# Optimization experiments

Measured on AMD Instinct MI355X. Metric: run time of the kernel, lower is better.

Reference implementation:

```python
import jax, jax.numpy as jnp
import numpy as np

N = 50000
E = 800000
IN_C, HID_C, OUT_C = 512, 128, 256


def setup_inputs() -> dict:
    key = jax.random.key(0)
    k1, k2, k3, k4, k5, k6 = jax.random.split(key, 6)
    x = jax.random.normal(k1, (N, IN_C), dtype=jnp.float32)
    edge_index = jax.random.randint(k2, (2, E), 0, N, dtype=jnp.int64)
    # Linear weights stored torch-style as [out, in]; bias per layer
    w1 = jax.random.normal(k3, (HID_C, IN_C), dtype=jnp.float32) * (1.0 / np.sqrt(IN_C))
    b1 = jax.random.normal(k4, (HID_C,), dtype=jnp.float32) * 0.02
    w2 = jax.random.normal(k5, (OUT_C, HID_C), dtype=jnp.float32) * (1.0 / np.sqrt(HID_C))
    b2 = jax.random.normal(k6, (OUT_C,), dtype=jnp.float32) * 0.02
    return {"x": x, "edge_index": edge_index, "w1": w1, "b1": b1, "w2": w2, "b2": b2}


def gcn_conv(x, edge_index, w, b):
    # x: [N, Cin], w: [Cout, Cin] (torch Linear layout), b: [Cout]
    h = x @ w.T                              # [N, Cout]
    src, dst = edge_index[0], edge_index[1]
    msgs = h[src]                            # gather: [E, Cout]
    agg = jax.ops.segment_sum(msgs, dst, num_segments=h.shape[0])  # scatter_add
    return agg + b


def reference(x, edge_index, w1, b1, w2, b2):
    h = gcn_conv(x, edge_index, w1, b1)
    h = jax.nn.relu(h)
    out = gcn_conv(h, edge_index, w2, b2)
    return out
```

## Files before the change

kernel.cpp:

```cpp
#include <hip/hip_runtime.h>

#define NN 50000
#define EE 800000
#define INC 512
#define HIDC 128
#define OUTC 256
#define CAP 64
#define OV_CAP 65536
#define BUILD_BLOCKS 196
#define GB1 782

typedef __attribute__((ext_vector_type(8))) short bf16x8;
typedef __attribute__((ext_vector_type(4))) float f32x4;

__device__ __forceinline__ short f2bf(float f) {
    unsigned u = __float_as_uint(f);
    unsigned r = u + 0x7fff + ((u >> 16) & 1);
    return (short)(r >> 16);
}
__device__ __forceinline__ float bf2f(short s) {
    return __uint_as_float(((unsigned)(unsigned short)s) << 16);
}

template<bool IN_BF16, bool ADDBIAS, bool OUT_BF16>
__device__ __forceinline__ void gemm_core(
    const void* __restrict__ Av, const float* __restrict__ B,
    const float* __restrict__ bias, void* __restrict__ Cv,
    int M, int Nc, int K, int bx, int by,
    short As[64][72], short Bs[128][72])
{
    int tid = threadIdx.x;
    int lane = tid & 63, wave = tid >> 6;
    int row0 = bx * 64, col0 = by * 128;
    int wm = (wave & 1) * 32, wn = (wave >> 1) * 64;
    int l16 = lane & 15, quad = lane >> 4;

    f32x4 acc[2][4];
#pragma unroll
    for (int i = 0; i < 2; i++)
#pragma unroll
        for (int j = 0; j < 4; j++) acc[i][j] = {0.f, 0.f, 0.f, 0.f};

    for (int k0 = 0; k0 < K; k0 += 64) {
        if (IN_BF16) {
            const short* A = (const short*)Av;
#pragma unroll
            for (int w = 0; w < 2; w++) {
                int f = tid + w * 256;
                int rr = f >> 3, c8 = f & 7;
                int gr = row0 + rr;
                bf16x8 v = {0, 0, 0, 0, 0, 0, 0, 0};
                if (gr < M) v = *(const bf16x8*)&A[(long)gr * K + k0 + c8 * 8];
                *(bf16x8*)&As[rr][c8 * 8] = v;
            }
        } else {
            const float* A = (const float*)Av;
#pragma unroll
            for (int w = 0; w < 4; w++) {
                int f = tid + w * 256;
                int rr = f >> 4, c4 = f & 15;
                int gr = row0 + rr;
                float4 v = make_float4(0.f, 0.f, 0.f, 0.f);
                if (gr < M) v = *(const float4*)&A[(long)gr * K + k0 + c4 * 4];
                short4 s;
                s.x = f2bf(v.x); s.y = f2bf(v.y); s.z = f2bf(v.z); s.w = f2bf(v.w);
                *(short4*)&As[rr][c4 * 4] = s;
            }
        }
#pragma unroll
        for (int w = 0; w < 8; w++) {
            int f = tid + w * 256;
            int rr = f >> 4, c4 = f & 15;
            float4 v = *(const float4*)&B[(long)(col0 + rr) * K + k0 + c4 * 4];
            short4 s;
            s.x = f2bf(v.x); s.y = f2bf(v.y); s.z = f2bf(v.z); s.w = f2bf(v.w);
            *(short4*)&Bs[rr][c4 * 4] = s;
        }
        __syncthreads();

#pragma unroll
        for (int kk = 0; kk < 64; kk += 32) {
            bf16x8 af[2], bfr[4];
#pragma unroll
            for (int i = 0; i < 2; i++)
                af[i] = *(const bf16x8*)&As[wm + i * 16 + l16][kk + quad * 8];
#pragma unroll
            for (int j = 0; j < 4; j++)
                bfr[j] = *(const bf16x8*)&Bs[wn + j * 16 + l16][kk + quad * 8];
#pragma unroll
            for (int i = 0; i < 2; i++)
#pragma unroll
                for (int j = 0; j < 4; j++)
                    acc[i][j] = __builtin_amdgcn_mfma_f32_16x16x32_bf16(
                        af[i], bfr[j], acc[i][j], 0, 0, 0);
        }
        __syncthreads();
    }

#pragma unroll
    for (int i = 0; i < 2; i++) {
#pragma unroll
        for (int rr = 0; rr < 4; rr++) {
            int grow = row0 + wm + i * 16 + quad * 4 + rr;
            if (grow < M) {
#pragma unroll
                for (int j = 0; j < 4; j++) {
                    int gcol = col0 + wn + j * 16 + l16;
                    float v = acc[i][j][rr];
                    if (ADDBIAS) v += bias[gcol];
                    if (OUT_BF16)
                        ((short*)Cv)[(long)grow * Nc + gcol] = f2bf(v);
                    else
                        ((float*)Cv)[(long)grow * Nc + gcol] = v;
                }
            }
        }
    }
}

__global__ __launch_bounds__(256) void fat_build_gemm1(
    const int* __restrict__ ei, int* __restrict__ cnt,
    unsigned short* __restrict__ bucket, int* __restrict__ ovcnt,
    int* __restrict__ ovlist,
    const float* __restrict__ x, const float* __restrict__ w1,
    short* __restrict__ h)
{
    __shared__ short As[64][72];
    __shared__ short Bs[128][72];

    if (blockIdx.x < BUILD_BLOCKS) {
        int t = threadIdx.x;
        long base = ((long)blockIdx.x * 256 + t) * 16;
        if (base + 16 <= EE) {
            int4 sv[4], dv[4];
#pragma unroll
            for (int q = 0; q < 4; q++) {
                sv[q] = *(const int4*)&ei[base + q * 4];
                dv[q] = *(const int4*)&ei[EE + base + q * 4];
            }
            const int* sp = (const int*)sv;
            const int* dp = (const int*)dv;
#pragma unroll
            for (int k = 0; k < 16; k++) {
                int src = sp[k], dst = dp[k];
                int pos = atomicAdd(&cnt[dst], 1);
                if (pos < CAP) bucket[(long)dst * CAP + pos] = (unsigned short)src;
                else {
                    int o = atomicAdd(ovcnt, 1);
                    if (o < OV_CAP) { ovlist[o * 2] = src; ovlist[o * 2 + 1] = dst; }
                }
            }
        } else {
            for (int k = 0; k < 16; k++) {
                long e = base + k;
                if (e < EE) {
                    int src = ei[e], dst = ei[EE + e];
                    int pos = atomicAdd(&cnt[dst], 1);
                    if (pos < CAP) bucket[(long)dst * CAP + pos] = (unsigned short)src;
                    else {
                        int o = atomicAdd(ovcnt, 1);
                        if (o < OV_CAP) { ovlist[o * 2] = src; ovlist[o * 2 + 1] = dst; }
                    }
                }
            }
        }
    } else {
        gemm_core<false, false, true>(x, w1, nullptr, h, NN, HIDC, INC,
                                      blockIdx.x - BUILD_BLOCKS, 0, As, Bs);
    }
}

__global__ __launch_bounds__(256) void gemm2_k(
    const short* __restrict__ r2, const float* __restrict__ w2,
    const float* __restrict__ b2, float* __restrict__ out)
{
    __shared__ short As[64][72];
    __shared__ short Bs[128][72];
    gemm_core<true, true, false>(r2, w2, b2, out, NN, OUTC, HIDC,
                                 blockIdx.x, blockIdx.y, As, Bs);
}

template<bool RELU>
__global__ __launch_bounds__(256) void gather_k(
    const short* __restrict__ hsrc, const unsigned short* __restrict__ bucket,
    const int* __restrict__ cnt, const float* __restrict__ bias,
    float* __restrict__ aggf, short* __restrict__ rout)
{
    int t = threadIdx.x;
    int node = blockIdx.x * 16 + (t >> 4);
    int c8 = t & 15;
    if (node >= NN) return;
    int m = cnt[node]; if (m > CAP) m = CAP;
    const unsigned short* bk = bucket + (long)node * CAP;
    float acc[8];
#pragma unroll
    for (int k = 0; k < 8; k++) acc[k] = 0.f;
    int j = 0;
    for (; j + 4 <= m; j += 4) {
        int s0 = bk[j], s1 = bk[j + 1], s2 = bk[j + 2], s3 = bk[j + 3];
        bf16x8 v0 = *(const bf16x8*)&hsrc[((long)s0 << 7) + c8 * 8];
        bf16x8 v1 = *(const bf16x8*)&hsrc[((long)s1 << 7) + c8 * 8];
        bf16x8 v2 = *(const bf16x8*)&hsrc[((long)s2 << 7) + c8 * 8];
        bf16x8 v3 = *(const bf16x8*)&hsrc[((long)s3 << 7) + c8 * 8];
#pragma unroll
        for (int k = 0; k < 8; k++)
            acc[k] += bf2f(v0[k]) + bf2f(v1[k]) + bf2f(v2[k]) + bf2f(v3[k]);
    }
    for (; j < m; j++) {
        int s0 = bk[j];
        bf16x8 v0 = *(const bf16x8*)&hsrc[((long)s0 << 7) + c8 * 8];
#pragma unroll
        for (int k = 0; k < 8; k++) acc[k] += bf2f(v0[k]);
    }
    if (RELU) {
        *(float4*)&aggf[((long)node << 7) + c8 * 8] =
            make_float4(acc[0], acc[1], acc[2], acc[3]);
        *(float4*)&aggf[((long)node << 7) + c8 * 8 + 4] =
            make_float4(acc[4], acc[5], acc[6], acc[7]);
        bf16x8 o;
#pragma unroll
        for (int k = 0; k < 8; k++)
            o[k] = f2bf(fmaxf(acc[k] + bias[c8 * 8 + k], 0.f));
        *(bf16x8*)&rout[((long)node << 7) + c8 * 8] = o;
    } else {
        bf16x8 o;
#pragma unroll
        for (int k = 0; k < 8; k++) o[k] = f2bf(acc[k]);
        *(bf16x8*)&rout[((long)node << 7) + c8 * 8] = o;
    }
}

__global__ __launch_bounds__(128) void ovfix1_k(
    const short* __restrict__ h, const float* __restrict__ b1,
    const int* __restrict__ ovcnt, const int* __restrict__ ovlist,
    float* __restrict__ agg1, short* __restrict__ r)
{
    int n = *ovcnt; if (n > OV_CAP) n = OV_CAP;
    int c = threadIdx.x;
    for (int i = 0; i < n; i++) {
        int src = ovlist[i * 2], dst = ovlist[i * 2 + 1];
        agg1[(long)dst * 128 + c] += bf2f(h[(long)src * 128 + c]);
    }
    __syncthreads();
    for (int i = 0; i < n; i++) {
        int dst = ovlist[i * 2 + 1];
        r[(long)dst * 128 + c] =
            f2bf(fmaxf(agg1[(long)dst * 128 + c] + b1[c], 0.f));
    }
}

__global__ __launch_bounds__(128) void ovfix2_k(
    const short* __restrict__ r, const unsigned short* __restrict__ bucket,
    const int* __restrict__ cnt, const int* __restrict__ ovcnt,
    const int* __restrict__ ovlist, short* __restrict__ r2)
{
    int n = *ovcnt; if (n > OV_CAP) n = OV_CAP;
    int c = threadIdx.x;
    for (int i = 0; i < n; i++) {
        int dst = ovlist[i * 2 + 1];
        bool dup = false;
        for (int i2 = 0; i2 < i; i2++)
            if (ovlist[i2 * 2 + 1] == dst) { dup = true; break; }
        if (dup) continue;
        int m = cnt[dst]; if (m > CAP) m = CAP;
        const unsigned short* bk = bucket + (long)dst * CAP;
        float acc = 0.f;
        for (int j = 0; j < m; j++)
            acc += bf2f(r[(long)bk[j] * 128 + c]);
        for (int i2 = 0; i2 < n; i2++)
            if (ovlist[i2 * 2 + 1] == dst)
                acc += bf2f(r[(long)ovlist[i2 * 2] * 128 + c]);
        r2[(long)dst * 128 + c] = f2bf(acc);
    }
}

extern "C" void kernel_launch(void* const* d_in, const int* in_sizes, int n_in,
                              void* d_out, int out_size, void* d_ws, size_t ws_size,
                              hipStream_t stream) {
    const float* x  = (const float*)d_in[0];
    const int*   ei = (const int*)d_in[1];
    const float* w1 = (const float*)d_in[2];
    const float* b1 = (const float*)d_in[3];
    const float* w2 = (const float*)d_in[4];
    const float* b2 = (const float*)d_in[5];
    float* out = (float*)d_out;

    char* ws = (char*)d_ws;
    size_t off = 0;
    short* h    = (short*)(ws + off); off += (size_t)NN * HIDC * 2;
    float* agg1 = (float*)(ws + off); off += (size_t)NN * HIDC * 4;
    short* r    = (short*)(ws + off); off += (size_t)NN * HIDC * 2;
    short* r2   = (short*)(ws + off); off += (size_t)NN * HIDC * 2;
    unsigned short* bucket = (unsigned short*)(ws + off);
    off += (size_t)NN * CAP * 2;
    int* cnt    = (int*)(ws + off);   off += (size_t)NN * 4;
    int* ovcnt  = (int*)(ws + off);   off += 256;
    int* ovlist = (int*)(ws + off);   off += (size_t)OV_CAP * 2 * 4;

    hipMemsetAsync(cnt, 0, (size_t)NN * 4 + 4, stream);

    dim3 blk(256);

    fat_build_gemm1<<<dim3(BUILD_BLOCKS + GB1), blk, 0, stream>>>(
        ei, cnt, bucket, ovcnt, ovlist, x, w1, h);

    gather_k<true><<<dim3(3125), blk, 0, stream>>>(h, bucket, cnt, b1, agg1, r);
    ovfix1_k<<<dim3(1), dim3(128), 0, stream>>>(h, b1, ovcnt, ovlist, agg1, r);

    gather_k<false><<<dim3(3125), blk, 0, stream>>>(r, bucket, cnt, nullptr, nullptr, r2);
    ovfix2_k<<<dim3(1), dim3(128), 0, stream>>>(r, bucket, cnt, ovcnt, ovlist, r2);

    gemm2_k<<<dim3(GB1, 2), blk, 0, stream>>>(r2, w2, b2, out);
}
```

Measured before the change: 297.2 us.

## Partition bucket build by destination slice per XCD and drop fp32 agg1 buffer

The edge bucket build now assigns each group of blocks (selected by blockIdx & 7, which is meant to map to one XCD) a slice of destination nodes. Each group scans all edges and only does atomics and bucket writes for its own slice, so the counter and bucket lines for a node stay in one XCD's L2 instead of bouncing between dies. The first gather no longer writes an fp32 aggregate. The overflow fixup instead recomputes full sums for overflowed nodes from the buckets plus the overflow list. In exchange, every edge index is read eight times, and the fixup does quadratic work in the overflow count.

After: 329.6 us. 10.9% more time.

```diff
diff --git a/kernel.cpp b/kernel.cpp
--- a/kernel.cpp
+++ b/kernel.cpp
@@ -7,7 +7,11 @@
 #define OUTC 256
 #define CAP 64
 #define OV_CAP 65536
-#define BUILD_BLOCKS 196
+#define BUILD_BLOCKS 192
+#define BLK_PER_XCD (BUILD_BLOCKS / 8)
+#define GRP_THREADS (BLK_PER_XCD * 256)
+#define NCHUNK (EE / 16)
+#define SLICE (NN / 8)
 #define GB1 782
 
 typedef __attribute__((ext_vector_type(8))) short bf16x8;
@@ -129,9 +133,12 @@
     __shared__ short Bs[128][72];
 
     if (blockIdx.x < BUILD_BLOCKS) {
-        int t = threadIdx.x;
-        long base = ((long)blockIdx.x * 256 + t) * 16;
-        if (base + 16 <= EE) {
+        int g = blockIdx.x & 7;
+        int rank = blockIdx.x >> 3;
+        int tig = rank * 256 + threadIdx.x;
+        int lo = g * SLICE;
+        for (int c = tig; c < NCHUNK; c += GRP_THREADS) {
+            long base = (long)c * 16;
             int4 sv[4], dv[4];
 #pragma unroll
             for (int q = 0; q < 4; q++) {
@@ -142,19 +149,9 @@
             const int* dp = (const int*)dv;
 #pragma unroll
             for (int k = 0; k < 16; k++) {
-                int src = sp[k], dst = dp[k];
-                int pos = atomicAdd(&cnt[dst], 1);
-                if (pos < CAP) bucket[(long)dst * CAP + pos] = (unsigned short)src;
-                else {
-                    int o = atomicAdd(ovcnt, 1);
-                    if (o < OV_CAP) { ovlist[o * 2] = src; ovlist[o * 2 + 1] = dst; }
-                }
-            }
-        } else {
-            for (int k = 0; k < 16; k++) {
-                long e = base + k;
-                if (e < EE) {
-                    int src = ei[e], dst = ei[EE + e];
+                int dst = dp[k];
+                if ((unsigned)(dst - lo) < SLICE) {
+                    int src = sp[k];
                     int pos = atomicAdd(&cnt[dst], 1);
                     if (pos < CAP) bucket[(long)dst * CAP + pos] = (unsigned short)src;
                     else {
@@ -184,7 +181,7 @@
 __global__ __launch_bounds__(256) void gather_k(
     const short* __restrict__ hsrc, const unsigned short* __restrict__ bucket,
     const int* __restrict__ cnt, const float* __restrict__ bias,
-    float* __restrict__ aggf, short* __restrict__ rout)
+    short* __restrict__ rout)
 {
     int t = threadIdx.x;
     int node = blockIdx.x * 16 + (t >> 4);
@@ -212,40 +209,41 @@
 #pragma unroll
         for (int k = 0; k < 8; k++) acc[k] += bf2f(v0[k]);
     }
+    bf16x8 o;
     if (RELU) {
-        *(float4*)&aggf[((long)node << 7) + c8 * 8] =
-            make_float4(acc[0], acc[1], acc[2], acc[3]);
-        *(float4*)&aggf[((long)node << 7) + c8 * 8 + 4] =
-            make_float4(acc[4], acc[5], acc[6], acc[7]);
-        bf16x8 o;
 #pragma unroll
         for (int k = 0; k < 8; k++)
             o[k] = f2bf(fmaxf(acc[k] + bias[c8 * 8 + k], 0.f));
-        *(bf16x8*)&rout[((long)node << 7) + c8 * 8] = o;
     } else {
-        bf16x8 o;
 #pragma unroll
         for (int k = 0; k < 8; k++) o[k] = f2bf(acc[k]);
-        *(bf16x8*)&rout[((long)node << 7) + c8 * 8] = o;
-    }
+    }
+    *(bf16x8*)&rout[((long)node << 7) + c8 * 8] = o;
 }
 
 __global__ __launch_bounds__(128) void ovfix1_k(
     const short* __restrict__ h, const float* __restrict__ b1,
+    const unsigned short* __restrict__ bucket, const int* __restrict__ cnt,
     const int* __restrict__ ovcnt, const int* __restrict__ ovlist,
-    float* __restrict__ agg1, short* __restrict__ r)
+    short* __restrict__ r)
 {
     int n = *ovcnt; if (n > OV_CAP) n = OV_CAP;
     int c = threadIdx.x;
     for (int i = 0; i < n; i++) {
-        int src = ovlist[i * 2], dst = ovlist[i * 2 + 1];
-        agg1[(long)dst * 128 + c] += bf2f(h[(long)src * 128 + c]);
-    }
-    __syncthreads();
-    for (int i = 0; i < n; i++) {
         int dst = ovlist[i * 2 + 1];
-        r[(long)dst * 128 + c] =
-            f2bf(fmaxf(agg1[(long)dst * 128 + c] + b1[c], 0.f));
+        bool dup = false;
+        for (int i2 = 0; i2 < i; i2++)
+            if (ovlist[i2 * 2 + 1] == dst) { dup = true; break; }
+        if (dup) continue;
+        int m = cnt[dst]; if (m > CAP) m = CAP;
+        const unsigned short* bk = bucket + (long)dst * CAP;
+        float acc = 0.f;
+        for (int j = 0; j < m; j++)
+            acc += bf2f(h[(long)bk[j] * 128 + c]);
+        for (int i2 = 0; i2 < n; i2++)
+            if (ovlist[i2 * 2 + 1] == dst)
+                acc += bf2f(h[(long)ovlist[i2 * 2] * 128 + c]);
+        r[(long)dst * 128 + c] = f2bf(fmaxf(acc + b1[c], 0.f));
     }
 }
 
@@ -288,7 +286,6 @@
     char* ws = (char*)d_ws;
     size_t off = 0;
     short* h    = (short*)(ws + off); off += (size_t)NN * HIDC * 2;
-    float* agg1 = (float*)(ws + off); off += (size_t)NN * HIDC * 4;
     short* r    = (short*)(ws + off); off += (size_t)NN * HIDC * 2;
     short* r2   = (short*)(ws + off); off += (size_t)NN * HIDC * 2;
     unsigned short* bucket = (unsigned short*)(ws + off);
@@ -304,10 +301,10 @@
     fat_build_gemm1<<<dim3(BUILD_BLOCKS + GB1), blk, 0, stream>>>(
         ei, cnt, bucket, ovcnt, ovlist, x, w1, h);
 
-    gather_k<true><<<dim3(3125), blk, 0, stream>>>(h, bucket, cnt, b1, agg1, r);
-    ovfix1_k<<<dim3(1), dim3(128), 0, stream>>>(h, b1, ovcnt, ovlist, agg1, r);
-
-    gather_k<false><<<dim3(3125), blk, 0, stream>>>(r, bucket, cnt, nullptr, nullptr, r2);
+    gather_k<true><<<dim3(3125), blk, 0, stream>>>(h, bucket, cnt, b1, r);
+    ovfix1_k<<<dim3(1), dim3(128), 0, stream>>>(h, b1, bucket, cnt, ovcnt, ovlist, r);
+
+    gather_k<false><<<dim3(3125), blk, 0, stream>>>(r, bucket, cnt, nullptr, r2);
     ovfix2_k<<<dim3(1), dim3(128), 0, stream>>>(r, bucket, cnt, ovcnt, ovlist, r2);
 
     gemm2_k<<<dim3(GB1, 2), blk, 0, stream>>>(r2, w2, b2, out);
```

## Fold overflow fixup into gather kernels and split edges across lane groups

Applied to the files above, without the earlier changes.

Rewrites the gather kernel so each wave handles four nodes sequentially. Within a node, four 16-lane subgroups split the edge list and are combined with xor shuffles. Nodes whose in-degree exceeds the bucket capacity now scan the overflow list inside the gather itself, which removes the two single-block serial fixup kernels and the fp32 agg1 intermediate write. The trade-off is a linear scan of the overflow list per overflowing node, plus extra shuffle work and fewer independent nodes per thread.

Measured after the change: 307.0 us (median of 2 runs). 1.03x slower.

```diff
diff --git a/kernel.cpp b/kernel.cpp
--- a/kernel.cpp
+++ b/kernel.cpp
@@ -183,94 +183,79 @@
 template<bool RELU>
 __global__ __launch_bounds__(256) void gather_k(
     const short* __restrict__ hsrc, const unsigned short* __restrict__ bucket,
-    const int* __restrict__ cnt, const float* __restrict__ bias,
-    float* __restrict__ aggf, short* __restrict__ rout)
-{
-    int t = threadIdx.x;
-    int node = blockIdx.x * 16 + (t >> 4);
-    int c8 = t & 15;
-    if (node >= NN) return;
-    int m = cnt[node]; if (m > CAP) m = CAP;
-    const unsigned short* bk = bucket + (long)node * CAP;
-    float acc[8];
-#pragma unroll
-    for (int k = 0; k < 8; k++) acc[k] = 0.f;
-    int j = 0;
-    for (; j + 4 <= m; j += 4) {
-        int s0 = bk[j], s1 = bk[j + 1], s2 = bk[j + 2], s3 = bk[j + 3];
-        bf16x8 v0 = *(const bf16x8*)&hsrc[((long)s0 << 7) + c8 * 8];
-        bf16x8 v1 = *(const bf16x8*)&hsrc[((long)s1 << 7) + c8 * 8];
-        bf16x8 v2 = *(const bf16x8*)&hsrc[((long)s2 << 7) + c8 * 8];
-        bf16x8 v3 = *(const bf16x8*)&hsrc[((long)s3 << 7) + c8 * 8];
-#pragma unroll
-        for (int k = 0; k < 8; k++)
-            acc[k] += bf2f(v0[k]) + bf2f(v1[k]) + bf2f(v2[k]) + bf2f(v3[k]);
-    }
-    for (; j < m; j++) {
-        int s0 = bk[j];
-        bf16x8 v0 = *(const bf16x8*)&hsrc[((long)s0 << 7) + c8 * 8];
-#pragma unroll
-        for (int k = 0; k < 8; k++) acc[k] += bf2f(v0[k]);
-    }
-    if (RELU) {
-        *(float4*)&aggf[((long)node << 7) + c8 * 8] =
-            make_float4(acc[0], acc[1], acc[2], acc[3]);
-        *(float4*)&aggf[((long)node << 7) + c8 * 8 + 4] =
-            make_float4(acc[4], acc[5], acc[6], acc[7]);
-        bf16x8 o;
-#pragma unroll
-        for (int k = 0; k < 8; k++)
-            o[k] = f2bf(fmaxf(acc[k] + bias[c8 * 8 + k], 0.f));
-        *(bf16x8*)&rout[((long)node << 7) + c8 * 8] = o;
-    } else {
-        bf16x8 o;
-#pragma unroll
-        for (int k = 0; k < 8; k++) o[k] = f2bf(acc[k]);
-        *(bf16x8*)&rout[((long)node << 7) + c8 * 8] = o;
-    }
-}
-
-__global__ __launch_bounds__(128) void ovfix1_k(
-    const short* __restrict__ h, const float* __restrict__ b1,
-    const int* __restrict__ ovcnt, const int* __restrict__ ovlist,
-    float* __restrict__ agg1, short* __restrict__ r)
-{
-    int n = *ovcnt; if (n > OV_CAP) n = OV_CAP;
-    int c = threadIdx.x;
-    for (int i = 0; i < n; i++) {
-        int src = ovlist[i * 2], dst = ovlist[i * 2 + 1];
-        agg1[(long)dst * 128 + c] += bf2f(h[(long)src * 128 + c]);
-    }
-    __syncthreads();
-    for (int i = 0; i < n; i++) {
-        int dst = ovlist[i * 2 + 1];
-        r[(long)dst * 128 + c] =
-            f2bf(fmaxf(agg1[(long)dst * 128 + c] + b1[c], 0.f));
-    }
-}
-
-__global__ __launch_bounds__(128) void ovfix2_k(
-    const short* __restrict__ r, const unsigned short* __restrict__ bucket,
     const int* __restrict__ cnt, const int* __restrict__ ovcnt,
-    const int* __restrict__ ovlist, short* __restrict__ r2)
-{
-    int n = *ovcnt; if (n > OV_CAP) n = OV_CAP;
-    int c = threadIdx.x;
-    for (int i = 0; i < n; i++) {
-        int dst = ovlist[i * 2 + 1];
-        bool dup = false;
-        for (int i2 = 0; i2 < i; i2++)
-            if (ovlist[i2 * 2 + 1] == dst) { dup = true; break; }
-        if (dup) continue;
-        int m = cnt[dst]; if (m > CAP) m = CAP;
-        const unsigned short* bk = bucket + (long)dst * CAP;
-        float acc = 0.f;
-        for (int j = 0; j < m; j++)
-            acc += bf2f(r[(long)bk[j] * 128 + c]);
-        for (int i2 = 0; i2 < n; i2++)
-            if (ovlist[i2 * 2 + 1] == dst)
-                acc += bf2f(r[(long)ovlist[i2 * 2] * 128 + c]);
-        r2[(long)dst * 128 + c] = f2bf(acc);
+    const int* __restrict__ ovlist, const float* __restrict__ bias,
+    short* __restrict__ rout)
+{
+    int wave = threadIdx.x >> 6;
+    int lane = threadIdx.x & 63;
+    int sub = lane >> 4, c8 = lane & 15;
+
+#pragma unroll
+    for (int it = 0; it < 4; it++) {
+        int node = blockIdx.x * 16 + wave * 4 + it;
+        int m0 = cnt[node];
+        int m = m0 > CAP ? CAP : m0;
+        const unsigned short* bk = bucket + (long)node * CAP;
+
+        float acc[8];
+#pragma unroll
+        for (int k = 0; k < 8; k++) acc[k] = 0.f;
+
+        int j = 0;
+        for (; j + 16 <= m; j += 16) {
+            int s0 = bk[j + sub];
+            int s1 = bk[j + 4 + sub];
+            int s2 = bk[j + 8 + sub];
+            int s3 = bk[j + 12 + sub];
+            bf16x8 v0 = *(const bf16x8*)&hsrc[((long)s0 << 7) + c8 * 8];
+            bf16x8 v1 = *(const bf16x8*)&hsrc[((long)s1 << 7) + c8 * 8];
+            bf16x8 v2 = *(const bf16x8*)&hsrc[((long)s2 << 7) + c8 * 8];
+            bf16x8 v3 = *(const bf16x8*)&hsrc[((long)s3 << 7) + c8 * 8];
+#pragma unroll
+            for (int k = 0; k < 8; k++)
+                acc[k] += bf2f(v0[k]) + bf2f(v1[k]) + bf2f(v2[k]) + bf2f(v3[k]);
+        }
+        for (; j < m; j += 4) {
+            int e = j + sub;
+            if (e < m) {
+                int s0 = bk[e];
+                bf16x8 v0 = *(const bf16x8*)&hsrc[((long)s0 << 7) + c8 * 8];
+#pragma unroll
+                for (int k = 0; k < 8; k++) acc[k] += bf2f(v0[k]);
+            }
+        }
+
+        if (m0 > CAP && sub == 0) {
+            int n = *ovcnt; if (n > OV_CAP) n = OV_CAP;
+            for (int i = 0; i < n; i++) {
+                if (ovlist[i * 2 + 1] == node) {
+                    bf16x8 v0 =
+                        *(const bf16x8*)&hsrc[((long)ovlist[i * 2] << 7) + c8 * 8];
+#pragma unroll
+                    for (int k = 0; k < 8; k++) acc[k] += bf2f(v0[k]);
+                }
+            }
+        }
+
+#pragma unroll
+        for (int k = 0; k < 8; k++) {
+            acc[k] += __shfl_xor(acc[k], 16);
+            acc[k] += __shfl_xor(acc[k], 32);
+        }
+
+        if (sub == 0) {
+            bf16x8 o;
+            if (RELU) {
+#pragma unroll
+                for (int k = 0; k < 8; k++)
+                    o[k] = f2bf(fmaxf(acc[k] + bias[c8 * 8 + k], 0.f));
+            } else {
+#pragma unroll
+                for (int k = 0; k < 8; k++) o[k] = f2bf(acc[k]);
+            }
+            *(bf16x8*)&rout[((long)node << 7) + c8 * 8] = o;
+        }
     }
 }
 
@@ -288,7 +273,6 @@
     char* ws = (char*)d_ws;
     size_t off = 0;
     short* h    = (short*)(ws + off); off += (size_t)NN * HIDC * 2;
-    float* agg1 = (float*)(ws + off); off += (size_t)NN * HIDC * 4;
     short* r    = (short*)(ws + off); off += (size_t)NN * HIDC * 2;
     short* r2   = (short*)(ws + off); off += (size_t)NN * HIDC * 2;
     unsigned short* bucket = (unsigned short*)(ws + off);
@@ -304,11 +288,11 @@
     fat_build_gemm1<<<dim3(BUILD_BLOCKS + GB1), blk, 0, stream>>>(
         ei, cnt, bucket, ovcnt, ovlist, x, w1, h);
 
-    gather_k<true><<<dim3(3125), blk, 0, stream>>>(h, bucket, cnt, b1, agg1, r);
-    ovfix1_k<<<dim3(1), dim3(128), 0, stream>>>(h, b1, ovcnt, ovlist, agg1, r);
-
-    gather_k<false><<<dim3(3125), blk, 0, stream>>>(r, bucket, cnt, nullptr, nullptr, r2);
-    ovfix2_k<<<dim3(1), dim3(128), 0, stream>>>(r, bucket, cnt, ovcnt, ovlist, r2);
+    gather_k<true><<<dim3(3125), blk, 0, stream>>>(
+        h, bucket, cnt, ovcnt, ovlist, b1, r);
+
+    gather_k<false><<<dim3(3125), blk, 0, stream>>>(
+        r, bucket, cnt, ovcnt, ovlist, nullptr, r2);
 
     gemm2_k<<<dim3(GB1, 2), blk, 0, stream>>>(r2, w2, b2, out);
 }
```
